# Optimization experiments

Measured on AMD Instinct MI355X. Metric: run time of the kernel, lower is better.

Reference implementation:

```python
import jax, jax.numpy as jnp
import numpy as np

N_NODES = 100000
N_EDGES = 1600000
N_GRAPHS = 64
IN_F, HID, OUT_F = 128, 256, 10


def setup_inputs() -> dict:
    key = jax.random.key(0)
    ks = jax.random.split(key, 9)
    x = jax.random.normal(ks[0], (N_NODES, IN_F), dtype=jnp.float32)
    edge_index = jax.random.randint(ks[1], (2, N_EDGES), 0, N_NODES, dtype=jnp.int64)
    batch = jnp.sort(jax.random.randint(ks[2], (N_NODES,), 0, N_GRAPHS, dtype=jnp.int64))
    # PyG GCNConv: lin (bias=False) weight [out, in], separate bias [out]
    def glorot(k, shape):
        lim = float(np.sqrt(6.0 / (shape[0] + shape[1])))
        return jax.random.uniform(k, shape, jnp.float32, -lim, lim)
    W1 = glorot(ks[3], (HID, IN_F));  b1 = jnp.zeros((HID,), jnp.float32)
    W2 = glorot(ks[4], (HID, HID));   b2 = jnp.zeros((HID,), jnp.float32)
    Wfc = glorot(ks[5], (OUT_F, HID))
    bfc = jax.random.uniform(ks[6], (OUT_F,), jnp.float32, -0.06, 0.06)
    return {"x": x, "edge_index": edge_index, "batch": batch,
            "W1": W1, "b1": b1, "W2": W2, "b2": b2, "Wfc": Wfc, "bfc": bfc}


def _gcn_norm(edge_index, n_nodes):
    # add self loops, compute symmetric normalization (PyG gcn_norm default)
    loop = jnp.arange(n_nodes, dtype=edge_index.dtype)
    src = jnp.concatenate([edge_index[0], loop])  # source j
    dst = jnp.concatenate([edge_index[1], loop])  # target i
    deg = jax.ops.segment_sum(jnp.ones_like(dst, jnp.float32), dst, num_segments=n_nodes)
    dinv = jnp.where(deg > 0, jax.lax.rsqrt(deg), 0.0)
    norm = dinv[src] * dinv[dst]  # [E+N]
    return src, dst, norm


def _gcn_conv(x, src, dst, norm, W, b, n_nodes):
    h = x @ W.T                                   # [N, out]
    msg = h[src] * norm[:, None]                  # gather + edge scale
    out = jax.ops.segment_sum(msg, dst, num_segments=n_nodes)  # scatter-add
    return out + b


def reference(x, edge_index, batch, W1, b1, W2, b2, Wfc, bfc):
    n = x.shape[0]
    src, dst, norm = _gcn_norm(edge_index, n)
    h = jax.nn.relu(_gcn_conv(x, src, dst, norm, W1, b1, n))
    h = jax.nn.relu(_gcn_conv(h, src, dst, norm, W2, b2, n))
    # global mean pool over graphs
    sums = jax.ops.segment_sum(h, batch, num_segments=N_GRAPHS)      # [G, HID]
    cnts = jax.ops.segment_sum(jnp.ones((n,), h.dtype), batch, num_segments=N_GRAPHS)
    pooled = sums / jnp.maximum(cnts, 1.0)[:, None]
    return pooled @ Wfc.T + bfc
```

## Files before the change

kernel.cpp:

```cpp
#include <hip/hip_runtime.h>

#define N_NODES 100000
#define N_EDGES 1600000
#define N_GRAPHS 64
#define IN_F 128
#define HID 256
#define OUT_F 10

#define SCAN_B 1024
#define SCAN_NB ((N_NODES + SCAN_B - 1) / SCAN_B)

typedef __attribute__((ext_vector_type(8))) short short8v;
typedef __attribute__((ext_vector_type(4))) float f32x4;

__device__ __forceinline__ unsigned short f2bf(float f) {
    unsigned int u = __float_as_uint(f);
    u += 0x7FFFu + ((u >> 16) & 1u);
    return (unsigned short)(u >> 16);
}
__device__ __forceinline__ float bf2f(unsigned short s) {
    return __uint_as_float((unsigned int)s << 16);
}

__global__ void k_count(const int* __restrict__ dst, int* __restrict__ cnt) {
    int e = blockIdx.x * blockDim.x + threadIdx.x;
    if (e < N_EDGES) atomicAdd(&cnt[dst[e]], 1);
}

__global__ void k_tobf2(const float* __restrict__ w1, unsigned short* __restrict__ w1b, int n1_8,
                        const float* __restrict__ w2, unsigned short* __restrict__ w2b, int n2_8) {
    int t = blockIdx.x * blockDim.x + threadIdx.x;
    const float* p;
    unsigned short* o;
    if (t < n1_8) { p = w1 + (size_t)t * 8; o = w1b + (size_t)t * 8; }
    else if (t < n1_8 + n2_8) { int u = t - n1_8; p = w2 + (size_t)u * 8; o = w2b + (size_t)u * 8; }
    else return;
    float4 a = *(const float4*)p;
    float4 b = *(const float4*)(p + 4);
    unsigned int o0 = f2bf(a.x) | ((unsigned int)f2bf(a.y) << 16);
    unsigned int o1 = f2bf(a.z) | ((unsigned int)f2bf(a.w) << 16);
    unsigned int o2 = f2bf(b.x) | ((unsigned int)f2bf(b.y) << 16);
    unsigned int o3 = f2bf(b.z) | ((unsigned int)f2bf(b.w) << 16);
    *(uint4*)o = make_uint4(o0, o1, o2, o3);
}

__global__ void k_xtobf(const float* __restrict__ x, const float* __restrict__ dinv,
                        unsigned short* __restrict__ xb) {
    int t = blockIdx.x * blockDim.x + threadIdx.x;
    if (t >= N_NODES * (IN_F / 8)) return;
    int node = t / (IN_F / 8);
    float sc = dinv[node];
    const float* p = x + (size_t)t * 8;
    float4 a = *(const float4*)p;
    float4 b = *(const float4*)(p + 4);
    unsigned int o0 = f2bf(a.x * sc) | ((unsigned int)f2bf(a.y * sc) << 16);
    unsigned int o1 = f2bf(a.z * sc) | ((unsigned int)f2bf(a.w * sc) << 16);
    unsigned int o2 = f2bf(b.x * sc) | ((unsigned int)f2bf(b.y * sc) << 16);
    unsigned int o3 = f2bf(b.z * sc) | ((unsigned int)f2bf(b.w * sc) << 16);
    *(uint4*)(xb + (size_t)t * 8) = make_uint4(o0, o1, o2, o3);
}

__global__ void k_scan1(const int* __restrict__ cnt, int* __restrict__ rowptr,
                        int* __restrict__ bsum, float* __restrict__ dinv) {
    __shared__ int sm[SCAN_B];
    int t = threadIdx.x, base = blockIdx.x * SCAN_B;
    int v = (base + t < N_NODES) ? cnt[base + t] : 0;
    if (base + t < N_NODES) dinv[base + t] = rsqrtf((float)v + 1.0f);
    int x = v;
    sm[t] = x;
    __syncthreads();
    for (int off = 1; off < SCAN_B; off <<= 1) {
        int add = (t >= off) ? sm[t - off] : 0;
        __syncthreads();
        x += add;
        sm[t] = x;
        __syncthreads();
    }
    if (base + t < N_NODES) rowptr[base + t] = x - v;
    if (t == SCAN_B - 1) bsum[blockIdx.x] = x;
}

__global__ void k_scan2(int* __restrict__ bsum) {
    __shared__ int sm[128];
    int t = threadIdx.x;
    int v = (t < SCAN_NB) ? bsum[t] : 0;
    int x = v;
    sm[t] = x;
    __syncthreads();
    for (int off = 1; off < 128; off <<= 1) {
        int add = (t >= off) ? sm[t - off] : 0;
        __syncthreads();
        x += add;
        sm[t] = x;
        __syncthreads();
    }
    if (t < SCAN_NB) bsum[t] = x - v;
}

__global__ void k_scan3(int* __restrict__ rowptr, const int* __restrict__ bsum) {
    int i = blockIdx.x * blockDim.x + threadIdx.x;
    if (i < N_NODES) rowptr[i] += bsum[i >> 10];
}

__global__ void k_fill(const int* __restrict__ src, const int* __restrict__ dst,
                       const int* __restrict__ rowptr, int* __restrict__ fill,
                       int* __restrict__ col) {
    int e = blockIdx.x * blockDim.x + threadIdx.x;
    if (e >= N_EDGES) return;
    int d = dst[e];
    int p = rowptr[d] + atomicAdd(&fill[d], 1);
    col[p] = src[e];
}

template<int W, int U>
__global__ void __launch_bounds__(256)
k_aggv(const unsigned short* __restrict__ hb, const float* __restrict__ dinv,
       const int* __restrict__ rowptr, const int* __restrict__ cnt,
       const int* __restrict__ col, unsigned short* __restrict__ out) {
    constexpr int LR = W / 8;
    constexpr int NW = 64 / LR;
    int wid = threadIdx.x >> 6;
    int i = blockIdx.x * 4 + wid;
    if (i >= N_NODES) return;
    int lane = threadIdx.x & 63;
    int g = lane / LR;
    int s = lane % LR;
    float dd = dinv[i];
    int beg = rowptr[i] - 1;
    int total = cnt[i] + 1;
    const unsigned short* hbs = hb + s * 8;
    float acc[8] = {};
    for (int v = 0; v < total; v += U * NW) {
        uint4 d[U];
        #pragma unroll
        for (int u = 0; u < U; ++u) {
            int idx = v + u * NW + g;
            d[u] = make_uint4(0u, 0u, 0u, 0u);
            if (idx < total) {
                int r = (idx == 0) ? i : col[beg + idx];
                d[u] = *(const uint4*)(hbs + (size_t)r * W);
            }
        }
        #pragma unroll
        for (int u = 0; u < U; ++u) {
            acc[0] += bf2f((unsigned short)(d[u].x & 0xffffu));
            acc[1] += bf2f((unsigned short)(d[u].x >> 16));
            acc[2] += bf2f((unsigned short)(d[u].y & 0xffffu));
            acc[3] += bf2f((unsigned short)(d[u].y >> 16));
            acc[4] += bf2f((unsigned short)(d[u].z & 0xffffu));
            acc[5] += bf2f((unsigned short)(d[u].z >> 16));
            acc[6] += bf2f((unsigned short)(d[u].w & 0xffffu));
            acc[7] += bf2f((unsigned short)(d[u].w >> 16));
        }
    }
    #pragma unroll
    for (int off = LR; off < 64; off <<= 1)
        #pragma unroll
        for (int c = 0; c < 8; ++c)
            acc[c] += __shfl_xor(acc[c], off, 64);
    if (g == 0) {
        unsigned int o0 = f2bf(dd * acc[0]) | ((unsigned int)f2bf(dd * acc[1]) << 16);
        unsigned int o1 = f2bf(dd * acc[2]) | ((unsigned int)f2bf(dd * acc[3]) << 16);
        unsigned int o2 = f2bf(dd * acc[4]) | ((unsigned int)f2bf(dd * acc[5]) << 16);
        unsigned int o3 = f2bf(dd * acc[6]) | ((unsigned int)f2bf(dd * acc[7]) << 16);
        *(uint4*)(out + (size_t)i * W + s * 8) = make_uint4(o0, o1, o2, o3);
    }
}

template<int K, bool FUSE>
__global__ void __launch_bounds__(256)
k_mgemm(const unsigned short* __restrict__ A, const unsigned short* __restrict__ Wb,
        const float* __restrict__ bias, unsigned short* __restrict__ Cb,
        const float* __restrict__ dinv, const int* __restrict__ batch,
        float* __restrict__ pooled) {
    constexpr int LDT = 72;
    __shared__ unsigned short Asl[128 * LDT];
    __shared__ unsigned short Bsl[128 * LDT];
    __shared__ float red[128];
    int row0 = blockIdx.x * 128;
    int col0 = blockIdx.y * 128;
    int t = threadIdx.x;
    int wid = t >> 6, lane = t & 63;
    int fr = lane & 15, fq = lane >> 4;
    int wr = wid >> 1, wc = wid & 1;

    f32x4 acc[4][4] = {};

    for (int kc = 0; kc < K; kc += 64) {
        #pragma unroll
        for (int p = 0; p < 4; ++p) {
            int idx = p * 256 + t;
            int r = idx >> 3;
            int c8 = (idx & 7) * 8;
            uint4 v = make_uint4(0u, 0u, 0u, 0u);
            int grow = row0 + r;
            if (grow < N_NODES) v = *(const uint4*)(A + (size_t)grow * K + kc + c8);
            *(uint4*)(Asl + r * LDT + c8) = v;
            uint4 w = *(const uint4*)(Wb + (size_t)(col0 + r) * K + kc + c8);
            *(uint4*)(Bsl + r * LDT + c8) = w;
        }
        __syncthreads();
        #pragma unroll
        for (int k0 = 0; k0 < 64; k0 += 32) {
            short8v af[4], bf[4];
            #pragma unroll
            for (int m = 0; m < 4; ++m)
                af[m] = *(const short8v*)(Asl + (wr * 64 + m * 16 + fr) * LDT + k0 + fq * 8);
            #pragma unroll
            for (int n = 0; n < 4; ++n)
                bf[n] = *(const short8v*)(Bsl + (wc * 64 + n * 16 + fr) * LDT + k0 + fq * 8);
            #pragma unroll
            for (int m = 0; m < 4; ++m)
                #pragma unroll
                for (int n = 0; n < 4; ++n)
                    acc[m][n] = __builtin_amdgcn_mfma_f32_16x16x32_bf16(af[m], bf[n], acc[m][n], 0, 0, 0);
        }
        __syncthreads();
    }

    float bv[4];
    #pragma unroll
    for (int n = 0; n < 4; ++n) bv[n] = bias[col0 + wc * 64 + n * 16 + fr];

    if (!FUSE) {
        #pragma unroll
        for (int m = 0; m < 4; ++m) {
            #pragma unroll
            for (int j = 0; j < 4; ++j) {
                int row = row0 + wr * 64 + m * 16 + fq * 4 + j;
                if (row >= N_NODES) continue;
                float sc = dinv[row];
                unsigned short* o = Cb + (size_t)row * HID + col0 + wc * 64;
                #pragma unroll
                for (int n = 0; n < 4; ++n) {
                    float v = fmaxf(acc[m][n][j] + bv[n], 0.f) * sc;
                    o[n * 16 + fr] = f2bf(v);
                }
            }
        }
    } else {
        int gm[4][4];
        #pragma unroll
        for (int m = 0; m < 4; ++m)
            #pragma unroll
            for (int j = 0; j < 4; ++j) {
                int row = row0 + wr * 64 + m * 16 + fq * 4 + j;
                gm[m][j] = (row < N_NODES) ? batch[row] : -1;
                #pragma unroll
                for (int n = 0; n < 4; ++n)
                    acc[m][n][j] = fmaxf(acc[m][n][j] + bv[n], 0.f);
            }
        int rhi = row0 + 127; if (rhi >= N_NODES) rhi = N_NODES - 1;
        int glo = batch[row0], ghi = batch[rhi];
        for (int g = glo; g <= ghi; ++g) {
            if (t < 128) red[t] = 0.f;
            __syncthreads();
            #pragma unroll
            for (int n = 0; n < 4; ++n) {
                float s = 0.f;
                #pragma unroll
                for (int m = 0; m < 4; ++m)
                    #pragma unroll
                    for (int j = 0; j < 4; ++j)
                        if (gm[m][j] == g) s += acc[m][n][j];
                if (s != 0.f) atomicAdd(&red[wc * 64 + n * 16 + fr], s);
            }
            __syncthreads();
            if (t < 128 && red[t] != 0.f)
                atomicAdd(&pooled[g * HID + col0 + t], red[t]);
            __syncthreads();
        }
    }
}

__global__ void k_final(const float* __restrict__ pooled, const int* __restrict__ batch,
                        const float* __restrict__ Wfc, const float* __restrict__ bfc,
                        float* __restrict__ out) {
    int t = blockIdx.x * blockDim.x + threadIdx.x;
    if (t >= N_GRAPHS * OUT_F) return;
    int g = t / OUT_F, o = t % OUT_F;
    int lo = 0, hi = N_NODES;
    while (lo < hi) { int mid = (lo + hi) >> 1; if (batch[mid] < g) lo = mid + 1; else hi = mid; }
    int a = lo;
    lo = 0; hi = N_NODES;
    while (lo < hi) { int mid = (lo + hi) >> 1; if (batch[mid] < g + 1) lo = mid + 1; else hi = mid; }
    float inv = 1.0f / fmaxf((float)(lo - a), 1.0f);
    float s = 0.f;
    for (int k = 0; k < HID; ++k) s += pooled[g * HID + k] * Wfc[o * HID + k];
    out[t] = s * inv + bfc[o];
}

extern "C" void kernel_launch(void* const* d_in, const int* in_sizes, int n_in,
                              void* d_out, int out_size, void* d_ws, size_t ws_size,
                              hipStream_t stream) {
    const float* x    = (const float*)d_in[0];
    const int*   ei   = (const int*)d_in[1];
    const int*   bat  = (const int*)d_in[2];
    const float* W1   = (const float*)d_in[3];
    const float* b1   = (const float*)d_in[4];
    const float* W2   = (const float*)d_in[5];
    const float* b2   = (const float*)d_in[6];
    const float* Wfc  = (const float*)d_in[7];
    const float* bfc  = (const float*)d_in[8];
    float* out = (float*)d_out;

    const int* src = ei;
    const int* dst = ei + N_EDGES;

    float* ws = (float*)d_ws;
    float* dinv    = ws + 0;
    float* pooled  = ws + 100096;
    float* cntg    = ws + 116480;
    int*   cnt     = (int*)(ws + 116608);
    int*   rowptr  = (int*)(ws + 216704);
    int*   fill    = (int*)(ws + 316928);
    int*   bsum    = (int*)(ws + 416928);
    int*   col     = (int*)(ws + 417056);
    unsigned short* W1b = (unsigned short*)(ws + 2017056);
    unsigned short* W2b = (unsigned short*)(ws + 2033440);
    unsigned short* xb  = (unsigned short*)(ws + 2066208);
    unsigned short* h1b = (unsigned short*)(ws + 8466208);
    unsigned short* aggb = (unsigned short*)(ws + 21266208);
    (void)cntg;

    const int B = 256;

    hipMemsetAsync(pooled, 0, (size_t)(417056 - 100096) * 4, stream);

    k_count<<<(N_EDGES + B - 1) / B, B, 0, stream>>>(dst, cnt);
    k_scan1<<<SCAN_NB, SCAN_B, 0, stream>>>(cnt, rowptr, bsum, dinv);
    k_scan2<<<1, 128, 0, stream>>>(bsum);
    k_scan3<<<(N_NODES + B - 1) / B, B, 0, stream>>>(rowptr, bsum);
    k_tobf2<<<((HID * IN_F + HID * HID) / 8 + B - 1) / B, B, 0, stream>>>(
        W1, W1b, HID * IN_F / 8, W2, W2b, HID * HID / 8);
    k_xtobf<<<(N_NODES * (IN_F / 8) + B - 1) / B, B, 0, stream>>>(x, dinv, xb);
    k_fill<<<(N_EDGES + B - 1) / B, B, 0, stream>>>(src, dst, rowptr, fill, col);

    k_aggv<IN_F, 4><<<(N_NODES + 3) / 4, 256, 0, stream>>>(xb, dinv, rowptr, cnt, col, aggb);
    {
        dim3 grid((N_NODES + 127) / 128, HID / 128);
        k_mgemm<IN_F, false><<<grid, 256, 0, stream>>>(aggb, W1b, b1, h1b, dinv, nullptr, nullptr);
    }

    k_aggv<HID, 4><<<(N_NODES + 3) / 4, 256, 0, stream>>>(h1b, dinv, rowptr, cnt, col, aggb);
    {
        dim3 grid((N_NODES + 127) / 128, HID / 128);
        k_mgemm<HID, true><<<grid, 256, 0, stream>>>(aggb, W2b, b2, nullptr, nullptr, bat, pooled);
    }

    k_final<<<(N_GRAPHS * OUT_F + B - 1) / B, B, 0, stream>>>(pooled, bat, Wfc, bfc, out);
}
```

Before: 470.1 us.

## Split aggregation feature columns by XCC half with atomic chunk queue

The gather-aggregate kernel now splits the feature dimension into two column slices. Blocks pull 128-node chunks from two atomic work queues, and each block picks its preferred queue from its XCC id so that each half of the XCDs mostly touches only one slice of the feature matrix. The aim is to cut the per-XCD L2 working set for the random neighbour gathers and so raise the cache hit rate. The cost is a block-level atomic plus a sync at the start of every block, and the queue counters must be zeroed by the existing memset range. The XCC-id mapping is also hardware specific.

New measurement: 545.4 us. 16.0% more time.

```diff
diff --git a/kernel.cpp b/kernel.cpp
--- a/kernel.cpp
+++ b/kernel.cpp
@@ -112,58 +112,73 @@
     col[p] = src[e];
 }
 
-template<int W, int U>
+template<int W, int SW, int U>
 __global__ void __launch_bounds__(256)
-k_aggv(const unsigned short* __restrict__ hb, const float* __restrict__ dinv,
+k_aggq(const unsigned short* __restrict__ hb, const float* __restrict__ dinv,
        const int* __restrict__ rowptr, const int* __restrict__ cnt,
-       const int* __restrict__ col, unsigned short* __restrict__ out) {
-    constexpr int LR = W / 8;
+       const int* __restrict__ col, unsigned short* __restrict__ out,
+       int* __restrict__ q, int nch) {
+    constexpr int LR = SW / 8;
     constexpr int NW = 64 / LR;
-    int wid = threadIdx.x >> 6;
-    int i = blockIdx.x * 4 + wid;
-    if (i >= N_NODES) return;
-    int lane = threadIdx.x & 63;
+    __shared__ int sh_c, sh_s;
+    if (threadIdx.x == 0) {
+        int xcc;
+        asm volatile("s_getreg_b32 %0, hwreg(HW_REG_XCC_ID)" : "=s"(xcc));
+        int pref = (xcc >> 2) & 1;
+        int c = atomicAdd(&q[pref], 1);
+        int sl = pref;
+        if (c >= nch) { c = atomicAdd(&q[1 ^ pref], 1); sl ^= 1; }
+        sh_c = c; sh_s = sl;
+    }
+    __syncthreads();
+    int chunk = sh_c, slice = sh_s;
+    if (chunk >= nch) return;
+    int wid = threadIdx.x >> 6, lane = threadIdx.x & 63;
     int g = lane / LR;
-    int s = lane % LR;
-    float dd = dinv[i];
-    int beg = rowptr[i] - 1;
-    int total = cnt[i] + 1;
-    const unsigned short* hbs = hb + s * 8;
-    float acc[8] = {};
-    for (int v = 0; v < total; v += U * NW) {
-        uint4 d[U];
-        #pragma unroll
-        for (int u = 0; u < U; ++u) {
-            int idx = v + u * NW + g;
-            d[u] = make_uint4(0u, 0u, 0u, 0u);
-            if (idx < total) {
-                int r = (idx == 0) ? i : col[beg + idx];
-                d[u] = *(const uint4*)(hbs + (size_t)r * W);
-            }
-        }
-        #pragma unroll
-        for (int u = 0; u < U; ++u) {
-            acc[0] += bf2f((unsigned short)(d[u].x & 0xffffu));
-            acc[1] += bf2f((unsigned short)(d[u].x >> 16));
-            acc[2] += bf2f((unsigned short)(d[u].y & 0xffffu));
-            acc[3] += bf2f((unsigned short)(d[u].y >> 16));
-            acc[4] += bf2f((unsigned short)(d[u].z & 0xffffu));
-            acc[5] += bf2f((unsigned short)(d[u].z >> 16));
-            acc[6] += bf2f((unsigned short)(d[u].w & 0xffffu));
-            acc[7] += bf2f((unsigned short)(d[u].w >> 16));
-        }
-    }
-    #pragma unroll
-    for (int off = LR; off < 64; off <<= 1)
-        #pragma unroll
-        for (int c = 0; c < 8; ++c)
-            acc[c] += __shfl_xor(acc[c], off, 64);
-    if (g == 0) {
-        unsigned int o0 = f2bf(dd * acc[0]) | ((unsigned int)f2bf(dd * acc[1]) << 16);
-        unsigned int o1 = f2bf(dd * acc[2]) | ((unsigned int)f2bf(dd * acc[3]) << 16);
-        unsigned int o2 = f2bf(dd * acc[4]) | ((unsigned int)f2bf(dd * acc[5]) << 16);
-        unsigned int o3 = f2bf(dd * acc[6]) | ((unsigned int)f2bf(dd * acc[7]) << 16);
-        *(uint4*)(out + (size_t)i * W + s * 8) = make_uint4(o0, o1, o2, o3);
+    int s8 = (lane % LR) * 8;
+    const unsigned short* hbs = hb + slice * SW + s8;
+    for (int it = 0; it < 32; ++it) {
+        int i = chunk * 128 + it * 4 + wid;
+        if (i >= N_NODES) break;
+        float dd = dinv[i];
+        int beg = rowptr[i] - 1;
+        int total = cnt[i] + 1;
+        float acc[8] = {};
+        for (int v = 0; v < total; v += U * NW) {
+            uint4 d[U];
+            #pragma unroll
+            for (int u = 0; u < U; ++u) {
+                int idx = v + u * NW + g;
+                d[u] = make_uint4(0u, 0u, 0u, 0u);
+                if (idx < total) {
+                    int r = (idx == 0) ? i : col[beg + idx];
+                    d[u] = *(const uint4*)(hbs + (size_t)r * W);
+                }
+            }
+            #pragma unroll
+            for (int u = 0; u < U; ++u) {
+                acc[0] += bf2f((unsigned short)(d[u].x & 0xffffu));
+                acc[1] += bf2f((unsigned short)(d[u].x >> 16));
+                acc[2] += bf2f((unsigned short)(d[u].y & 0xffffu));
+                acc[3] += bf2f((unsigned short)(d[u].y >> 16));
+                acc[4] += bf2f((unsigned short)(d[u].z & 0xffffu));
+                acc[5] += bf2f((unsigned short)(d[u].z >> 16));
+                acc[6] += bf2f((unsigned short)(d[u].w & 0xffffu));
+                acc[7] += bf2f((unsigned short)(d[u].w >> 16));
+            }
+        }
+        #pragma unroll
+        for (int off = LR; off < 64; off <<= 1)
+            #pragma unroll
+            for (int c = 0; c < 8; ++c)
+                acc[c] += __shfl_xor(acc[c], off, 64);
+        if (g == 0) {
+            unsigned int o0 = f2bf(dd * acc[0]) | ((unsigned int)f2bf(dd * acc[1]) << 16);
+            unsigned int o1 = f2bf(dd * acc[2]) | ((unsigned int)f2bf(dd * acc[3]) << 16);
+            unsigned int o2 = f2bf(dd * acc[4]) | ((unsigned int)f2bf(dd * acc[5]) << 16);
+            unsigned int o3 = f2bf(dd * acc[6]) | ((unsigned int)f2bf(dd * acc[7]) << 16);
+            *(uint4*)(out + (size_t)i * W + slice * SW + s8) = make_uint4(o0, o1, o2, o3);
+        }
     }
 }
 
@@ -310,18 +325,18 @@
     float* ws = (float*)d_ws;
     float* dinv    = ws + 0;
     float* pooled  = ws + 100096;
-    float* cntg    = ws + 116480;
     int*   cnt     = (int*)(ws + 116608);
     int*   rowptr  = (int*)(ws + 216704);
     int*   fill    = (int*)(ws + 316928);
     int*   bsum    = (int*)(ws + 416928);
+    int*   q1      = (int*)(ws + 417040);
+    int*   q2      = (int*)(ws + 417048);
     int*   col     = (int*)(ws + 417056);
     unsigned short* W1b = (unsigned short*)(ws + 2017056);
     unsigned short* W2b = (unsigned short*)(ws + 2033440);
     unsigned short* xb  = (unsigned short*)(ws + 2066208);
     unsigned short* h1b = (unsigned short*)(ws + 8466208);
     unsigned short* aggb = (unsigned short*)(ws + 21266208);
-    (void)cntg;
 
     const int B = 256;
 
@@ -336,13 +351,15 @@
     k_xtobf<<<(N_NODES * (IN_F / 8) + B - 1) / B, B, 0, stream>>>(x, dinv, xb);
     k_fill<<<(N_EDGES + B - 1) / B, B, 0, stream>>>(src, dst, rowptr, fill, col);
 
-    k_aggv<IN_F, 4><<<(N_NODES + 3) / 4, 256, 0, stream>>>(xb, dinv, rowptr, cnt, col, aggb);
+    const int NCH = (N_NODES + 127) / 128;
+
+    k_aggq<IN_F, 64, 4><<<2 * NCH, 256, 0, stream>>>(xb, dinv, rowptr, cnt, col, aggb, q1, NCH);
     {
         dim3 grid((N_NODES + 127) / 128, HID / 128);
         k_mgemm<IN_F, false><<<grid, 256, 0, stream>>>(aggb, W1b, b1, h1b, dinv, nullptr, nullptr);
     }
 
-    k_aggv<HID, 4><<<(N_NODES + 3) / 4, 256, 0, stream>>>(h1b, dinv, rowptr, cnt, col, aggb);
+    k_aggq<HID, 128, 4><<<2 * NCH, 256, 0, stream>>>(h1b, dinv, rowptr, cnt, col, aggb, q2, NCH);
     {
         dim3 grid((N_NODES + 127) / 128, HID / 128);
         k_mgemm<HID, true><<<grid, 256, 0, stream>>>(aggb, W2b, b2, nullptr, nullptr, bat, pooled);
```

## Use 8-wave GEMM blocks with register prefetch of next K tile

Applied to the files above, without the earlier changes.

The MFMA GEMM block grows from 4 to 8 waves, each wave now covering 32 rows instead of 64, which halves per-thread accumulators. Global loads for the next 64-wide K chunk are issued into registers before the current chunk's MFMAs and stored to shared memory afterwards. The goal is to overlap global latency with compute and raise occupancy. The cost is extra synchronization per K step and a fixed shared-memory footprint per larger block.

Measured after the change: 480.9 us. +2.3%, slower.

```diff
diff --git a/kernel.cpp b/kernel.cpp
--- a/kernel.cpp
+++ b/kernel.cpp
@@ -168,12 +168,13 @@
 }
 
 template<int K, bool FUSE>
-__global__ void __launch_bounds__(256)
+__global__ void __launch_bounds__(512)
 k_mgemm(const unsigned short* __restrict__ A, const unsigned short* __restrict__ Wb,
         const float* __restrict__ bias, unsigned short* __restrict__ Cb,
         const float* __restrict__ dinv, const int* __restrict__ batch,
         float* __restrict__ pooled) {
     constexpr int LDT = 72;
+    constexpr int NT = K / 64;
     __shared__ unsigned short Asl[128 * LDT];
     __shared__ unsigned short Bsl[128 * LDT];
     __shared__ float red[128];
@@ -184,38 +185,62 @@
     int fr = lane & 15, fq = lane >> 4;
     int wr = wid >> 1, wc = wid & 1;
 
-    f32x4 acc[4][4] = {};
-
-    for (int kc = 0; kc < K; kc += 64) {
-        #pragma unroll
-        for (int p = 0; p < 4; ++p) {
-            int idx = p * 256 + t;
-            int r = idx >> 3;
-            int c8 = (idx & 7) * 8;
-            uint4 v = make_uint4(0u, 0u, 0u, 0u);
-            int grow = row0 + r;
-            if (grow < N_NODES) v = *(const uint4*)(A + (size_t)grow * K + kc + c8);
-            *(uint4*)(Asl + r * LDT + c8) = v;
-            uint4 w = *(const uint4*)(Wb + (size_t)(col0 + r) * K + kc + c8);
-            *(uint4*)(Bsl + r * LDT + c8) = w;
-        }
-        __syncthreads();
+    f32x4 acc[2][4] = {};
+    uint4 ra[2], rb[2];
+
+    #pragma unroll
+    for (int p = 0; p < 2; ++p) {
+        int idx = p * 512 + t, r = idx >> 3, c8 = (idx & 7) * 8;
+        int grow = row0 + r;
+        ra[p] = make_uint4(0u, 0u, 0u, 0u);
+        if (grow < N_NODES) ra[p] = *(const uint4*)(A + (size_t)grow * K + c8);
+        rb[p] = *(const uint4*)(Wb + (size_t)(col0 + r) * K + c8);
+    }
+    #pragma unroll
+    for (int p = 0; p < 2; ++p) {
+        int idx = p * 512 + t, r = idx >> 3, c8 = (idx & 7) * 8;
+        *(uint4*)(Asl + r * LDT + c8) = ra[p];
+        *(uint4*)(Bsl + r * LDT + c8) = rb[p];
+    }
+    __syncthreads();
+
+    for (int tt = 0; tt < NT; ++tt) {
+        if (tt + 1 < NT) {
+            int kc = (tt + 1) * 64;
+            #pragma unroll
+            for (int p = 0; p < 2; ++p) {
+                int idx = p * 512 + t, r = idx >> 3, c8 = (idx & 7) * 8;
+                int grow = row0 + r;
+                ra[p] = make_uint4(0u, 0u, 0u, 0u);
+                if (grow < N_NODES) ra[p] = *(const uint4*)(A + (size_t)grow * K + kc + c8);
+                rb[p] = *(const uint4*)(Wb + (size_t)(col0 + r) * K + kc + c8);
+            }
+        }
         #pragma unroll
         for (int k0 = 0; k0 < 64; k0 += 32) {
-            short8v af[4], bf[4];
-            #pragma unroll
-            for (int m = 0; m < 4; ++m)
-                af[m] = *(const short8v*)(Asl + (wr * 64 + m * 16 + fr) * LDT + k0 + fq * 8);
+            short8v af[2], bf[4];
+            #pragma unroll
+            for (int m = 0; m < 2; ++m)
+                af[m] = *(const short8v*)(Asl + (wr * 32 + m * 16 + fr) * LDT + k0 + fq * 8);
             #pragma unroll
             for (int n = 0; n < 4; ++n)
                 bf[n] = *(const short8v*)(Bsl + (wc * 64 + n * 16 + fr) * LDT + k0 + fq * 8);
             #pragma unroll
-            for (int m = 0; m < 4; ++m)
+            for (int m = 0; m < 2; ++m)
                 #pragma unroll
                 for (int n = 0; n < 4; ++n)
                     acc[m][n] = __builtin_amdgcn_mfma_f32_16x16x32_bf16(af[m], bf[n], acc[m][n], 0, 0, 0);
         }
         __syncthreads();
+        if (tt + 1 < NT) {
+            #pragma unroll
+            for (int p = 0; p < 2; ++p) {
+                int idx = p * 512 + t, r = idx >> 3, c8 = (idx & 7) * 8;
+                *(uint4*)(Asl + r * LDT + c8) = ra[p];
+                *(uint4*)(Bsl + r * LDT + c8) = rb[p];
+            }
+            __syncthreads();
+        }
     }
 
     float bv[4];
@@ -224,10 +249,10 @@
 
     if (!FUSE) {
         #pragma unroll
-        for (int m = 0; m < 4; ++m) {
+        for (int m = 0; m < 2; ++m) {
             #pragma unroll
             for (int j = 0; j < 4; ++j) {
-                int row = row0 + wr * 64 + m * 16 + fq * 4 + j;
+                int row = row0 + wr * 32 + m * 16 + fq * 4 + j;
                 if (row >= N_NODES) continue;
                 float sc = dinv[row];
                 unsigned short* o = Cb + (size_t)row * HID + col0 + wc * 64;
@@ -239,12 +264,12 @@
             }
         }
     } else {
-        int gm[4][4];
-        #pragma unroll
-        for (int m = 0; m < 4; ++m)
+        int gm[2][4];
+        #pragma unroll
+        for (int m = 0; m < 2; ++m)
             #pragma unroll
             for (int j = 0; j < 4; ++j) {
-                int row = row0 + wr * 64 + m * 16 + fq * 4 + j;
+                int row = row0 + wr * 32 + m * 16 + fq * 4 + j;
                 gm[m][j] = (row < N_NODES) ? batch[row] : -1;
                 #pragma unroll
                 for (int n = 0; n < 4; ++n)
@@ -259,7 +284,7 @@
             for (int n = 0; n < 4; ++n) {
                 float s = 0.f;
                 #pragma unroll
-                for (int m = 0; m < 4; ++m)
+                for (int m = 0; m < 2; ++m)
                     #pragma unroll
                     for (int j = 0; j < 4; ++j)
                         if (gm[m][j] == g) s += acc[m][n][j];
@@ -310,7 +335,6 @@
     float* ws = (float*)d_ws;
     float* dinv    = ws + 0;
     float* pooled  = ws + 100096;
-    float* cntg    = ws + 116480;
     int*   cnt     = (int*)(ws + 116608);
     int*   rowptr  = (int*)(ws + 216704);
     int*   fill    = (int*)(ws + 316928);
@@ -321,7 +345,6 @@
     unsigned short* xb  = (unsigned short*)(ws + 2066208);
     unsigned short* h1b = (unsigned short*)(ws + 8466208);
     unsigned short* aggb = (unsigned short*)(ws + 21266208);
-    (void)cntg;
 
     const int B = 256;
 
@@ -339,13 +362,13 @@
     k_aggv<IN_F, 4><<<(N_NODES + 3) / 4, 256, 0, stream>>>(xb, dinv, rowptr, cnt, col, aggb);
     {
         dim3 grid((N_NODES + 127) / 128, HID / 128);
-        k_mgemm<IN_F, false><<<grid, 256, 0, stream>>>(aggb, W1b, b1, h1b, dinv, nullptr, nullptr);
+        k_mgemm<IN_F, false><<<grid, 512, 0, stream>>>(aggb, W1b, b1, h1b, dinv, nullptr, nullptr);
     }
 
     k_aggv<HID, 4><<<(N_NODES + 3) / 4, 256, 0, stream>>>(h1b, dinv, rowptr, cnt, col, aggb);
     {
         dim3 grid((N_NODES + 127) / 128, HID / 128);
-        k_mgemm<HID, true><<<grid, 256, 0, stream>>>(aggb, W2b, b2, nullptr, nullptr, bat, pooled);
+        k_mgemm<HID, true><<<grid, 512, 0, stream>>>(aggb, W2b, b2, nullptr, nullptr, bat, pooled);
     }
 
     k_final<<<(N_GRAPHS * OUT_F + B - 1) / B, B, 0, stream>>>(pooled, bat, Wfc, bfc, out);
```
